# Kernel tuning notes

Measured on AMD Instinct MI355X. Metric: run time of the kernel, lower is better.

Reference implementation:

```python
import jax, jax.numpy as jnp
import numpy as np
import math

B, S, D = 2, 2048, 1024
H = 16
DK = D // H  # dim_k == dim_v == 64


def setup_inputs() -> dict:
    key = jax.random.key(0)
    ks = jax.random.split(key, 8)
    scale = 1.0 / math.sqrt(D)
    inp = {
        "query": jax.random.normal(ks[0], (B, S, D), dtype=jnp.float32),
        "key": jax.random.normal(ks[1], (B, S, D), dtype=jnp.float32),
        "value": jax.random.normal(ks[2], (B, S, D), dtype=jnp.float32),
        # stacked per-head projection weights (torch Linear y = x @ W.T; here stored as [H, D, DK])
        "Wq": jax.random.uniform(ks[3], (H, D, DK), dtype=jnp.float32, minval=-scale, maxval=scale),
        "Wk": jax.random.uniform(ks[4], (H, D, DK), dtype=jnp.float32, minval=-scale, maxval=scale),
        "Wv": jax.random.uniform(ks[5], (H, D, DK), dtype=jnp.float32, minval=-scale, maxval=scale),
        "Wo": jax.random.uniform(ks[6], (D, H * DK), dtype=jnp.float32, minval=-scale, maxval=scale),
        "bo": jax.random.uniform(ks[7], (D,), dtype=jnp.float32, minval=-scale, maxval=scale),
    }
    return inp


def reference(query, key, value, Wq, Wk, Wv, Wo, bo):
    # per-head projections, batched over heads via einsum
    q = jnp.einsum("bsd,hdk->bhsk", query, Wq)   # [B,H,S,DK]
    k = jnp.einsum("btd,hdk->bhtk", key, Wk)     # [B,H,S,DK]
    v = jnp.einsum("btd,hdv->bhtv", value, Wv)   # [B,H,S,DK]
    scores = jnp.einsum("bhsk,bhtk->bhst", q, k) / jnp.sqrt(jnp.float32(DK))
    # causal mask (is_causal=True): strictly upper triangle -> -inf
    causal = jnp.tril(jnp.ones((S, S), dtype=bool))  # True = keep
    scores = jnp.where(causal[None, None], scores, -jnp.inf)
    attn = jax.nn.softmax(scores, axis=-1)
    # NaN correction (no-op under pure causal masking, kept for faithfulness)
    attn = jnp.where(jnp.isnan(attn), 0.0, attn)
    out = jnp.einsum("bhst,bhtv->bhsv", attn, v)  # [B,H,S,DK]
    out = jnp.transpose(out, (0, 2, 1, 3)).reshape(B, S, H * DK)  # concat heads
    return out @ Wo.T + bo
```

## Files before the change

### kernel.cpp

```cpp
#include <hip/hip_runtime.h>


#define B_ 2
#define S_ 2048
#define D_ 1024
#define H_ 16
#define DK_ 64
#define NEG_BIG (-1e30f)

typedef unsigned short u16;
typedef __attribute__((ext_vector_type(8))) short bf16x8;
typedef __attribute__((ext_vector_type(4))) float f32x4;

__device__ __forceinline__ float b2f(u16 v) {
    union { unsigned u; float f; } x; x.u = ((unsigned)v) << 16; return x.f;
}
__device__ __forceinline__ u16 f2b(float f) {
    union { float f; unsigned u; } x; x.f = f;
    unsigned r = x.u + 0x7fff + ((x.u >> 16) & 1);
    return (u16)(r >> 16);
}

__device__ __forceinline__ bool is_f32(const void* p) {
    const unsigned* u = (const unsigned*)p;
    int cnt = 0;
#pragma unroll
    for (int i = 0; i < 64; i++) {
        unsigned e = (u[i * 8] >> 7) & 0xFFu;
        cnt += (e >= 110u && e <= 134u) ? 1 : 0;
    }
    return cnt < 32;
}

template<bool F32>
__device__ __forceinline__ bf16x8 load8(const void* p, size_t idx) {
    if constexpr (F32) {
        const float* f = (const float*)p + idx;
        float4 a = *(const float4*)f;
        float4 b = *(const float4*)(f + 4);
        bf16x8 r;
        ((u16*)&r)[0] = f2b(a.x); ((u16*)&r)[1] = f2b(a.y);
        ((u16*)&r)[2] = f2b(a.z); ((u16*)&r)[3] = f2b(a.w);
        ((u16*)&r)[4] = f2b(b.x); ((u16*)&r)[5] = f2b(b.y);
        ((u16*)&r)[6] = f2b(b.z); ((u16*)&r)[7] = f2b(b.w);
        return r;
    } else {
        return *(const bf16x8*)((const u16*)p + idx);
    }
}

__global__ __launch_bounds__(256) void wtrans(const void* Wq, const void* Wk, const void* Wv,
                                              u16* WqT, u16* WkT, u16* WvT) {
    __shared__ __align__(16) u16 Ts[64][72];
    const int t = threadIdx.x;
    const int k0 = blockIdx.x * 64;
    const int h = blockIdx.y;
    const int wsel = blockIdx.z;
    const void* W = (wsel == 0) ? Wq : (wsel == 1) ? Wk : Wv;
    u16* WT = (wsel == 0) ? WqT : (wsel == 1) ? WkT : WvT;
    const bool wf = is_f32(W);

    const int drow = t >> 2, c0 = (t & 3) * 16;
    size_t sidx = ((size_t)h * D_ + k0 + drow) * DK_ + c0;
    bf16x8 v0, v1;
    if (wf) { v0 = load8<true >(W, sidx); v1 = load8<true >(W, sidx + 8); }
    else    { v0 = load8<false>(W, sidx); v1 = load8<false>(W, sidx + 8); }
    *(bf16x8*)&Ts[drow][c0]     = v0;
    *(bf16x8*)&Ts[drow][c0 + 8] = v1;
    __syncthreads();

    const int nrow = t >> 2, kc0 = (t & 3) * 16;
    u16 tmp[16];
#pragma unroll
    for (int j = 0; j < 16; j++) tmp[j] = Ts[kc0 + j][nrow];
    u16* dst = &WT[((size_t)h * DK_ + nrow) * D_ + k0 + kc0];
    *(bf16x8*)&dst[0] = *(const bf16x8*)&tmp[0];
    *(bf16x8*)&dst[8] = *(const bf16x8*)&tmp[8];
}

template<bool AF32>
__device__ void qproj_body(const void* A, const u16* WT, u16* Qt, int bb,
                           u16 (*As)[72], u16 (*Wt)[72]) {
    const int tid = threadIdx.x, mt = blockIdx.x, h = blockIdx.y;
    const int w = tid >> 6, lane = tid & 63, quad = lane >> 4, ln = lane & 15;
    const int s0 = mt * 64;
    const int row = tid >> 3, col = (tid & 7) * 8;
    const int row1 = row + 32;
    const int brow = tid >> 2, bc0 = (tid & 3) * 16;
    const size_t wbase = ((size_t)h * DK_ + brow) * D_ + bc0;

    bf16x8 areg0, areg1, breg0, breg1;
    areg0 = load8<AF32>(A, ((size_t)bb * S_ + s0 + row ) * D_ + col);
    areg1 = load8<AF32>(A, ((size_t)bb * S_ + s0 + row1) * D_ + col);
    breg0 = *(const bf16x8*)&WT[wbase];
    breg1 = *(const bf16x8*)&WT[wbase + 8];

    f32x4 acc[4];
#pragma unroll
    for (int t = 0; t < 4; t++)
#pragma unroll
        for (int r = 0; r < 4; r++) acc[t][r] = 0.f;

    for (int k0 = 0; k0 < D_; k0 += 64) {
        *(bf16x8*)&As[row ][col] = areg0;
        *(bf16x8*)&As[row1][col] = areg1;
        *(bf16x8*)&Wt[brow][bc0    ] = breg0;
        *(bf16x8*)&Wt[brow][bc0 + 8] = breg1;
        __syncthreads();
        if (k0 + 64 < D_) {
            areg0 = load8<AF32>(A, ((size_t)bb * S_ + s0 + row ) * D_ + k0 + 64 + col);
            areg1 = load8<AF32>(A, ((size_t)bb * S_ + s0 + row1) * D_ + k0 + 64 + col);
            breg0 = *(const bf16x8*)&WT[wbase + k0 + 64];
            breg1 = *(const bf16x8*)&WT[wbase + k0 + 64 + 8];
        }
#pragma unroll
        for (int kk = 0; kk < 2; kk++) {
            bf16x8 a = *(const bf16x8*)&As[w * 16 + ln][kk * 32 + quad * 8];
#pragma unroll
            for (int t = 0; t < 4; t++) {
                bf16x8 bm = *(const bf16x8*)&Wt[t * 16 + ln][kk * 32 + quad * 8];
                acc[t] = __builtin_amdgcn_mfma_f32_16x16x32_bf16(a, bm, acc[t], 0, 0, 0);
            }
        }
        __syncthreads();
    }

#pragma unroll
    for (int t = 0; t < 4; t++)
#pragma unroll
        for (int r = 0; r < 4; r++)
            Qt[((size_t)bb * S_ + s0 + w * 16 + quad * 4 + r) * D_ + h * DK_ + t * 16 + ln] =
                f2b(acc[t][r] * 0.125f);
}

__global__ __launch_bounds__(256) void qproj(const void* query, const u16* WqT, u16* Qt) {
    __shared__ __align__(16) u16 As[64][72];
    __shared__ __align__(16) u16 Wt[64][72];
    const int bb = blockIdx.z;
    if (is_f32(query)) qproj_body<true >(query, WqT, Qt, bb, As, Wt);
    else               qproj_body<false>(query, WqT, Qt, bb, As, Wt);
}

template<bool AF32>
__device__ void projkv_body(const void* A, const u16* WT, u16* Ko, u16* VTo,
                            int bb, int which, u16 (*As)[72], u16 (*Wt)[72]) {
    const int tid = threadIdx.x, mt = blockIdx.x, h = blockIdx.y;
    const int w = tid >> 6, lane = tid & 63, quad = lane >> 4, ln = lane & 15;
    const int s0 = mt * 64;
    const int row = tid >> 3, col = (tid & 7) * 8;
    const int row1 = row + 32;
    const int brow = tid >> 2, bc0 = (tid & 3) * 16;
    const size_t wbase = ((size_t)h * DK_ + brow) * D_ + bc0;

    bf16x8 areg0, areg1, breg0, breg1;
    areg0 = load8<AF32>(A, ((size_t)bb * S_ + s0 + row ) * D_ + col);
    areg1 = load8<AF32>(A, ((size_t)bb * S_ + s0 + row1) * D_ + col);
    breg0 = *(const bf16x8*)&WT[wbase];
    breg1 = *(const bf16x8*)&WT[wbase + 8];

    f32x4 acc[4];
#pragma unroll
    for (int t = 0; t < 4; t++)
#pragma unroll
        for (int r = 0; r < 4; r++) acc[t][r] = 0.f;

    for (int k0 = 0; k0 < D_; k0 += 64) {
        *(bf16x8*)&As[row ][col] = areg0;
        *(bf16x8*)&As[row1][col] = areg1;
        *(bf16x8*)&Wt[brow][bc0    ] = breg0;
        *(bf16x8*)&Wt[brow][bc0 + 8] = breg1;
        __syncthreads();
        if (k0 + 64 < D_) {
            areg0 = load8<AF32>(A, ((size_t)bb * S_ + s0 + row ) * D_ + k0 + 64 + col);
            areg1 = load8<AF32>(A, ((size_t)bb * S_ + s0 + row1) * D_ + k0 + 64 + col);
            breg0 = *(const bf16x8*)&WT[wbase + k0 + 64];
            breg1 = *(const bf16x8*)&WT[wbase + k0 + 64 + 8];
        }
#pragma unroll
        for (int kk = 0; kk < 2; kk++) {
            bf16x8 a = *(const bf16x8*)&As[w * 16 + ln][kk * 32 + quad * 8];
#pragma unroll
            for (int t = 0; t < 4; t++) {
                bf16x8 bm = *(const bf16x8*)&Wt[t * 16 + ln][kk * 32 + quad * 8];
                acc[t] = __builtin_amdgcn_mfma_f32_16x16x32_bf16(a, bm, acc[t], 0, 0, 0);
            }
        }
        __syncthreads();
    }

    if (which == 0) {
#pragma unroll
        for (int t = 0; t < 4; t++)
#pragma unroll
            for (int r = 0; r < 4; r++)
                Ko[((size_t)h * S_ + s0 + w * 16 + quad * 4 + r) * DK_ + t * 16 + ln] =
                    f2b(acc[t][r]);
    } else {
#pragma unroll
        for (int t = 0; t < 4; t++)
#pragma unroll
            for (int r = 0; r < 4; r++)
                Wt[t * 16 + ln][w * 16 + quad * 4 + r] = f2b(acc[t][r]);
        __syncthreads();
        *(bf16x8*)&VTo[((size_t)h * DK_ + row ) * S_ + s0 + col] = *(const bf16x8*)&Wt[row ][col];
        *(bf16x8*)&VTo[((size_t)h * DK_ + row1) * S_ + s0 + col] = *(const bf16x8*)&Wt[row1][col];
    }
}

__global__ __launch_bounds__(256) void projkv(const void* key, const void* value,
                                              const u16* WkT, const u16* WvT,
                                              u16* Ko, u16* VTo, int bb) {
    __shared__ __align__(16) u16 As[64][72];
    __shared__ __align__(16) u16 Wt[64][72];
    const int which = blockIdx.z;
    const void* A = which ? value : key;
    const u16* WT = which ? WvT : WkT;
    if (is_f32(A)) projkv_body<true >(A, WT, Ko, VTo, bb, which, As, Wt);
    else           projkv_body<false>(A, WT, Ko, VTo, bb, which, As, Wt);
}

__global__ __launch_bounds__(256) void flashq(u16* __restrict__ Xq,
                                              const u16* __restrict__ Kb,
                                              const u16* __restrict__ VTb, int bb) {
    __shared__ __align__(16) u16 BufA[64][72];
    __shared__ __align__(16) u16 BufB[64][72];
    __shared__ __align__(16) u16 Ps[4][16][72];
    const int tid = threadIdx.x;
    const int qt = (int)(gridDim.x - 1 - blockIdx.x);
    const int h = blockIdx.y;
    const int w = tid >> 6, lane = tid & 63, quad = lane >> 4, ln = lane & 15;
    const int s0 = qt * 64;
    const int row = tid >> 3, col = (tid & 7) * 8;
    const int row1 = row + 32;

    bf16x8 kreg0, kreg1, vreg0, vreg1;
    kreg0 = *(const bf16x8*)&Kb [((size_t)h * S_  + row ) * DK_ + col];
    kreg1 = *(const bf16x8*)&Kb [((size_t)h * S_  + row1) * DK_ + col];
    vreg0 = *(const bf16x8*)&VTb[((size_t)h * DK_ + row ) * S_  + col];
    vreg1 = *(const bf16x8*)&VTb[((size_t)h * DK_ + row1) * S_  + col];

    *(bf16x8*)&BufA[row ][col] = *(const bf16x8*)&Xq[((size_t)bb * S_ + s0 + row ) * D_ + h * DK_ + col];
    *(bf16x8*)&BufA[row1][col] = *(const bf16x8*)&Xq[((size_t)bb * S_ + s0 + row1) * D_ + h * DK_ + col];
    __syncthreads();
    bf16x8 qa0 = *(const bf16x8*)&BufA[w * 16 + ln][quad * 8];
    bf16x8 qa1 = *(const bf16x8*)&BufA[w * 16 + ln][32 + quad * 8];
    __syncthreads();

    f32x4 O[4];
    float psum[4];
#pragma unroll
    for (int t = 0; t < 4; t++)
#pragma unroll
        for (int r = 0; r < 4; r++) O[t][r] = 0.f;
#pragma unroll
    for (int r = 0; r < 4; r++) psum[r] = 0.f;

    for (int j = 0; j <= qt; j++) {
        *(bf16x8*)&BufA[row ][col] = kreg0;
        *(bf16x8*)&BufA[row1][col] = kreg1;
        *(bf16x8*)&BufB[row ][col] = vreg0;
        *(bf16x8*)&BufB[row1][col] = vreg1;
        __syncthreads();

        if (j < qt) {
            kreg0 = *(const bf16x8*)&Kb [((size_t)h * S_  + (j + 1) * 64 + row ) * DK_ + col];
            kreg1 = *(const bf16x8*)&Kb [((size_t)h * S_  + (j + 1) * 64 + row1) * DK_ + col];
            vreg0 = *(const bf16x8*)&VTb[((size_t)h * DK_ + row ) * S_ + (j + 1) * 64 + col];
            vreg1 = *(const bf16x8*)&VTb[((size_t)h * DK_ + row1) * S_ + (j + 1) * 64 + col];
        }

        f32x4 sf[4];
#pragma unroll
        for (int t = 0; t < 4; t++)
#pragma unroll
            for (int r = 0; r < 4; r++) sf[t][r] = 0.f;
#pragma unroll
        for (int kk = 0; kk < 2; kk++) {
            bf16x8 a = kk ? qa1 : qa0;
#pragma unroll
            for (int t = 0; t < 4; t++) {
                bf16x8 bm = *(const bf16x8*)&BufA[t * 16 + ln][kk * 32 + quad * 8];
                sf[t] = __builtin_amdgcn_mfma_f32_16x16x32_bf16(a, bm, sf[t], 0, 0, 0);
            }
        }

        if (j == qt) {
#pragma unroll
            for (int t = 0; t < 4; t++) {
                int keyl = t * 16 + ln;
#pragma unroll
                for (int r = 0; r < 4; r++) {
                    int qr = w * 16 + quad * 4 + r;
                    if (keyl > qr) sf[t][r] = NEG_BIG;
                }
            }
        }

#pragma unroll
        for (int t = 0; t < 4; t++)
#pragma unroll
            for (int r = 0; r < 4; r++) {
                float p = __expf(sf[t][r]);
                psum[r] += p;
                Ps[w][quad * 4 + r][t * 16 + ln] = f2b(p);
            }
        __syncthreads();

#pragma unroll
        for (int kk = 0; kk < 2; kk++) {
            bf16x8 a = *(const bf16x8*)&Ps[w][ln][kk * 32 + quad * 8];
#pragma unroll
            for (int t = 0; t < 4; t++) {
                bf16x8 bm = *(const bf16x8*)&BufB[t * 16 + ln][kk * 32 + quad * 8];
                O[t] = __builtin_amdgcn_mfma_f32_16x16x32_bf16(a, bm, O[t], 0, 0, 0);
            }
        }
        __syncthreads();
    }

#pragma unroll
    for (int r = 0; r < 4; r++) {
        float s = psum[r];
        s += __shfl_xor(s, 1, 64);
        s += __shfl_xor(s, 2, 64);
        s += __shfl_xor(s, 4, 64);
        s += __shfl_xor(s, 8, 64);
        float inv = 1.0f / s;
        int sr = s0 + w * 16 + quad * 4 + r;
#pragma unroll
        for (int t = 0; t < 4; t++) {
            Xq[((size_t)bb * S_ + sr) * D_ + h * DK_ + t * 16 + ln] = f2b(O[t][r] * inv);
        }
    }
}

__global__ __launch_bounds__(256) void copyx(const u16* __restrict__ src,
                                             u16* __restrict__ dst) {
    size_t i = ((size_t)blockIdx.x * 256 + threadIdx.x) * 8;
    *(bf16x8*)&dst[i] = *(const bf16x8*)&src[i];
}

template<bool WF32>
__device__ void outgemm_body(const u16* X, const void* Wo, const void* bo, bool bf32,
                             float* Y, u16 (*As)[72], u16 (*Bs)[72]) {
    const int tid = threadIdx.x, mt = blockIdx.x, nt = blockIdx.y;
    const int w = tid >> 6, lane = tid & 63, quad = lane >> 4, ln = lane & 15;
    const int m0 = mt * 64, n0 = nt * 64;
    const int row = tid >> 3, col = (tid & 7) * 8;
    const int row1 = row + 32;

    bf16x8 areg0, areg1, wreg0, wreg1;
    areg0 = *(const bf16x8*)&X[(size_t)(m0 + row ) * D_ + col];
    areg1 = *(const bf16x8*)&X[(size_t)(m0 + row1) * D_ + col];
    wreg0 = load8<WF32>(Wo, (size_t)(n0 + row ) * D_ + col);
    wreg1 = load8<WF32>(Wo, (size_t)(n0 + row1) * D_ + col);

    f32x4 acc[4];
#pragma unroll
    for (int t = 0; t < 4; t++)
#pragma unroll
        for (int r = 0; r < 4; r++) acc[t][r] = 0.f;

    for (int k0 = 0; k0 < D_; k0 += 64) {
        *(bf16x8*)&As[row ][col] = areg0;
        *(bf16x8*)&As[row1][col] = areg1;
        *(bf16x8*)&Bs[row ][col] = wreg0;
        *(bf16x8*)&Bs[row1][col] = wreg1;
        __syncthreads();
        if (k0 + 64 < D_) {
            areg0 = *(const bf16x8*)&X[(size_t)(m0 + row ) * D_ + k0 + 64 + col];
            areg1 = *(const bf16x8*)&X[(size_t)(m0 + row1) * D_ + k0 + 64 + col];
            wreg0 = load8<WF32>(Wo, (size_t)(n0 + row ) * D_ + k0 + 64 + col);
            wreg1 = load8<WF32>(Wo, (size_t)(n0 + row1) * D_ + k0 + 64 + col);
        }
#pragma unroll
        for (int kk = 0; kk < 2; kk++) {
            bf16x8 a = *(const bf16x8*)&As[w * 16 + ln][kk * 32 + quad * 8];
#pragma unroll
            for (int t = 0; t < 4; t++) {
                bf16x8 bm = *(const bf16x8*)&Bs[t * 16 + ln][kk * 32 + quad * 8];
                acc[t] = __builtin_amdgcn_mfma_f32_16x16x32_bf16(a, bm, acc[t], 0, 0, 0);
            }
        }
        __syncthreads();
    }

#pragma unroll
    for (int t = 0; t < 4; t++) {
        int n = n0 + t * 16 + ln;
        float bias = bf32 ? ((const float*)bo)[n] : b2f(((const u16*)bo)[n]);
#pragma unroll
        for (int r = 0; r < 4; r++) {
            int m = m0 + w * 16 + quad * 4 + r;
            Y[(size_t)m * D_ + n] = acc[t][r] + bias;
        }
    }
}

__global__ __launch_bounds__(256) void outgemm(const u16* __restrict__ X,
                                               const void* Wo, const void* bo,
                                               float* __restrict__ Y) {
    __shared__ __align__(16) u16 As[64][72];
    __shared__ __align__(16) u16 Bs[64][72];
    const bool wf = is_f32(Wo), bf = is_f32(bo);
    if (wf) outgemm_body<true >(X, Wo, bo, bf, Y, As, Bs);
    else    outgemm_body<false>(X, Wo, bo, bf, Y, As, Bs);
}

extern "C" void kernel_launch(void* const* d_in, const int* in_sizes, int n_in,
                              void* d_out, int out_size, void* d_ws, size_t ws_size,
                              hipStream_t stream) {
    const void* q  = d_in[0];
    const void* k  = d_in[1];
    const void* v  = d_in[2];
    const void* Wq = d_in[3];
    const void* Wk = d_in[4];
    const void* Wv = d_in[5];
    const void* Wo = d_in[6];
    const void* bo = d_in[7];

    u16* ob   = (u16*)d_out;
    u16* Xq   = ob;
    u16* WkT  = ob + (size_t)4 * 1024 * 1024;
    u16* WvT  = WkT + (size_t)1024 * 1024;
    u16* WqT  = WvT + (size_t)1024 * 1024;
    u16* ws16 = (u16*)d_ws;
    const size_t halfkv = (size_t)H_ * S_ * DK_;
    u16* Kw  = ws16;
    u16* VTw = ws16 + halfkv;

    wtrans<<<dim3(D_ / 64, H_, 3), dim3(256), 0, stream>>>(Wq, Wk, Wv, WqT, WkT, WvT);
    qproj<<<dim3(S_ / 64, H_, B_), dim3(256), 0, stream>>>(q, WqT, Xq);
    for (int bb = 0; bb < B_; bb++) {
        projkv<<<dim3(S_ / 64, H_, 2), dim3(256), 0, stream>>>(k, v, WkT, WvT, Kw, VTw, bb);
        flashq<<<dim3(S_ / 64, H_), dim3(256), 0, stream>>>(Xq, Kw, VTw, bb);
    }
    copyx<<<dim3((B_ * S_ * D_) / (256 * 8)), dim3(256), 0, stream>>>(Xq, ws16);
    outgemm<<<dim3((B_ * S_) / 64, D_ / 64), dim3(256), 0, stream>>>(ws16, Wo, bo, (float*)d_out);
}
```

Before: 318.3 us.

## Batch both flash-attention batches into one launch when workspace allows

When the workspace holds at least 16M u16 elements, K/V projections for both batches go into separate workspace regions, so a single flashq launch with a z-dimension of 2 covers both batches. This doubles the blocks per attention launch and removes one serialized launch, improving occupancy on the causal-skewed grid. It also swaps the round-to-nearest-even bf16 conversion of softmax probabilities for a cheaper round-half-up, with a slight change in rounding. A fallback path keeps the old per-batch sequence when the workspace is small.

```diff
diff --git a/kernel.cpp b/kernel.cpp
--- a/kernel.cpp
+++ b/kernel.cpp
@@ -19,6 +19,10 @@
     union { float f; unsigned u; } x; x.f = f;
     unsigned r = x.u + 0x7fff + ((x.u >> 16) & 1);
     return (u16)(r >> 16);
+}
+__device__ __forceinline__ u16 f2b_fast(float f) {
+    union { float f; unsigned u; } x; x.f = f;
+    return (u16)((x.u + 0x8000u) >> 16);
 }
 
 __device__ __forceinline__ bool is_f32(const void* p) {
@@ -209,25 +213,30 @@
 
 __global__ __launch_bounds__(256) void projkv(const void* key, const void* value,
                                               const u16* WkT, const u16* WvT,
-                                              u16* Ko, u16* VTo, int bb) {
+                                              u16* KVbase, int bb) {
     __shared__ __align__(16) u16 As[64][72];
     __shared__ __align__(16) u16 Wt[64][72];
     const int which = blockIdx.z;
     const void* A = which ? value : key;
     const u16* WT = which ? WvT : WkT;
+    u16* Ko  = KVbase;
+    u16* VTo = KVbase + (size_t)H_ * S_ * DK_;
     if (is_f32(A)) projkv_body<true >(A, WT, Ko, VTo, bb, which, As, Wt);
     else           projkv_body<false>(A, WT, Ko, VTo, bb, which, As, Wt);
 }
 
 __global__ __launch_bounds__(256) void flashq(u16* __restrict__ Xq,
-                                              const u16* __restrict__ Kb,
-                                              const u16* __restrict__ VTb, int bb) {
+                                              const u16* __restrict__ KV,
+                                              int bb0, size_t zstride) {
     __shared__ __align__(16) u16 BufA[64][72];
     __shared__ __align__(16) u16 BufB[64][72];
     __shared__ __align__(16) u16 Ps[4][16][72];
     const int tid = threadIdx.x;
     const int qt = (int)(gridDim.x - 1 - blockIdx.x);
     const int h = blockIdx.y;
+    const int bb = bb0 + blockIdx.z;
+    const u16* Kb  = KV + (size_t)blockIdx.z * zstride;
+    const u16* VTb = Kb + (size_t)H_ * S_ * DK_;
     const int w = tid >> 6, lane = tid & 63, quad = lane >> 4, ln = lane & 15;
     const int s0 = qt * 64;
     const int row = tid >> 3, col = (tid & 7) * 8;
@@ -302,7 +311,7 @@
             for (int r = 0; r < 4; r++) {
                 float p = __expf(sf[t][r]);
                 psum[r] += p;
-                Ps[w][quad * 4 + r][t * 16 + ln] = f2b(p);
+                Ps[w][quad * 4 + r][t * 16 + ln] = f2b_fast(p);
             }
         __syncthreads();
 
@@ -425,15 +434,20 @@
     u16* WvT  = WkT + (size_t)1024 * 1024;
     u16* WqT  = WvT + (size_t)1024 * 1024;
     u16* ws16 = (u16*)d_ws;
-    const size_t halfkv = (size_t)H_ * S_ * DK_;
-    u16* Kw  = ws16;
-    u16* VTw = ws16 + halfkv;
+    const size_t kvblk = (size_t)2 * H_ * S_ * DK_;
+    const bool bigws = ws_size >= (size_t)16 * 1024 * 1024;
 
     wtrans<<<dim3(D_ / 64, H_, 3), dim3(256), 0, stream>>>(Wq, Wk, Wv, WqT, WkT, WvT);
     qproj<<<dim3(S_ / 64, H_, B_), dim3(256), 0, stream>>>(q, WqT, Xq);
-    for (int bb = 0; bb < B_; bb++) {
-        projkv<<<dim3(S_ / 64, H_, 2), dim3(256), 0, stream>>>(k, v, WkT, WvT, Kw, VTw, bb);
-        flashq<<<dim3(S_ / 64, H_), dim3(256), 0, stream>>>(Xq, Kw, VTw, bb);
+    if (bigws) {
+        projkv<<<dim3(S_ / 64, H_, 2), dim3(256), 0, stream>>>(k, v, WkT, WvT, ws16, 0);
+        projkv<<<dim3(S_ / 64, H_, 2), dim3(256), 0, stream>>>(k, v, WkT, WvT, ws16 + kvblk, 1);
+        flashq<<<dim3(S_ / 64, H_, 2), dim3(256), 0, stream>>>(Xq, ws16, 0, kvblk);
+    } else {
+        projkv<<<dim3(S_ / 64, H_, 2), dim3(256), 0, stream>>>(k, v, WkT, WvT, ws16, 0);
+        flashq<<<dim3(S_ / 64, H_, 1), dim3(256), 0, stream>>>(Xq, ws16, 0, 0);
+        projkv<<<dim3(S_ / 64, H_, 2), dim3(256), 0, stream>>>(k, v, WkT, WvT, ws16, 1);
+        flashq<<<dim3(S_ / 64, H_, 1), dim3(256), 0, stream>>>(Xq, ws16, 1, 0);
     }
     copyx<<<dim3((B_ * S_ * D_) / (256 * 8)), dim3(256), 0, stream>>>(Xq, ws16);
     outgemm<<<dim3((B_ * S_) / 64, D_ / 64), dim3(256), 0, stream>>>(ws16, Wo, bo, (float*)d_out);
```

Result: faster. 291.4 us (-8.5%).
